# Kernel tuning notes

Measured on AMD Instinct MI355X. Metric: run time of the kernel, lower is better.

## Reference

```python
import jax, jax.numpy as jnp
import numpy as np

LATENT = 2000
N_GROUPS = 10000  # loci_count // window_size
KERNEL = 20       # window_size * 2; per-group input length is 1 so out length == KERNEL
BATCH = 128
EPS = 1e-5
SLOPE = 0.1


def setup_inputs() -> dict:
    key = jax.random.key(0)
    k1, k2, k3, k4, k5 = jax.random.split(key, 5)
    return {
        "z": jax.random.normal(k1, (BATCH, LATENT), dtype=jnp.float32),
        "W_fc": jax.random.normal(k2, (N_GROUPS, LATENT), dtype=jnp.float32) * 0.02,
        "b_fc": jax.random.normal(k3, (N_GROUPS,), dtype=jnp.float32) * 0.02,
        "gamma": jnp.ones((N_GROUPS,), dtype=jnp.float32),
        "beta": jnp.zeros((N_GROUPS,), dtype=jnp.float32),
        "conv_w": jax.random.normal(k4, (N_GROUPS, KERNEL), dtype=jnp.float32) * 0.1,
        "conv_b": jax.random.normal(k5, (N_GROUPS,), dtype=jnp.float32) * 0.02,
    }


def reference(z, W_fc, b_fc, gamma, beta, conv_w, conv_b):
    # Linear: (B, L) @ (L, G) -> (B, G)
    h = jnp.einsum("bl,gl->bg", z, W_fc) + b_fc
    # BatchNorm1d (training mode: biased batch statistics, eps=1e-5)
    mean = jnp.mean(h, axis=0)
    var = jnp.mean(jnp.square(h - mean), axis=0)
    h = (h - mean) * jax.lax.rsqrt(var + EPS) * gamma + beta
    h = jnp.where(h >= 0, h, SLOPE * h)  # LeakyReLU(0.1)
    # Grouped ConvTranspose1d with per-group input length 1 degenerates to
    # an outer product per channel: y[b,g,k] = h[b,g]*w[g,k] + b[g]
    y = h[:, :, None] * conv_w[None, :, :] + conv_b[None, :, None]  # (B, G, K)
    y = jnp.where(y >= 0, y, SLOPE * y)  # LeakyReLU(0.1)
    out = jax.nn.sigmoid(y.reshape(z.shape[0], N_GROUPS * KERNEL))
    return out
```

## Files before the change

### kernel.cpp

```cpp
#include <hip/hip_runtime.h>
#include <hip/hip_bf16.h>
#include <stdint.h>

#define BATCH 128
#define LAT   2000
#define NG    10000
#define KW    20
#define OUTW  (NG * KW)
#define EPSV  1e-5f

#define GT    64
#define BK    64
#define KSPL  8
#define KSEG  256

typedef __bf16 bf16x8 __attribute__((ext_vector_type(8)));
typedef float  f32x4  __attribute__((ext_vector_type(4)));

__device__ __forceinline__ ushort f2bf(float f) {
  uint32_t u = __builtin_bit_cast(uint32_t, f);
  u = (u + 0x7FFFu + ((u >> 16) & 1u)) >> 16;
  return (ushort)u;
}

__device__ __forceinline__ int4 pack8(const float* p) {
  float4 f0 = *(const float4*)p;
  float4 f1 = *(const float4*)(p + 4);
  int4 v;
  v.x = (int)((uint32_t)f2bf(f0.x) | ((uint32_t)f2bf(f0.y) << 16));
  v.y = (int)((uint32_t)f2bf(f0.z) | ((uint32_t)f2bf(f0.w) << 16));
  v.z = (int)((uint32_t)f2bf(f1.x) | ((uint32_t)f2bf(f1.y) << 16));
  v.w = (int)((uint32_t)f2bf(f1.z) | ((uint32_t)f2bf(f1.w) << 16));
  return v;
}

__global__ __launch_bounds__(256, 4) void convert_z_kernel(
    const float* __restrict__ zp, ushort* __restrict__ zb) {
  const int idx = (blockIdx.x * 256 + threadIdx.x) * 8;
  int4 v = pack8(zp + idx);
  *(int4*)(zb + idx) = v;
}

__global__ __launch_bounds__(256, 4) void gemm_splitk_kernel(
    const ushort* __restrict__ zb, const float* __restrict__ wp,
    float* __restrict__ hp) {
  const int tid = threadIdx.x;
  const int g0  = blockIdx.x * GT;
  const int s   = blockIdx.y;
  const int kbase = s * KSEG;
  const int klen  = (s < KSPL - 1) ? KSEG : (LAT - (KSPL - 1) * KSEG);

  __shared__ ushort As[GT * BK];
  __shared__ ushort Bs[BATCH * BK];

  const int lane = tid & 63;
  const int w    = tid >> 6;
  const int wm   = w & 1;
  const int wn   = w >> 1;
  const int q    = lane >> 4;
  const int cl   = lane & 15;

  f32x4 acc[2][4];
  const f32x4 vzero = {0.f, 0.f, 0.f, 0.f};
#pragma unroll
  for (int i = 0; i < 2; ++i)
#pragma unroll
    for (int j = 0; j < 4; ++j) acc[i][j] = vzero;

  for (int it = 0; it < KSEG / BK; ++it) {
    const int k0 = it * BK;
    __syncthreads();

#pragma unroll
    for (int i = 0; i < 2; ++i) {
      int c = i * 256 + tid;
      int r = c >> 3, sc = c & 7;
      int lk = k0 + sc * 8;
      int g  = g0 + r;
      int4 v = make_int4(0, 0, 0, 0);
      if (lk < klen && g < NG)
        v = pack8(wp + (size_t)g * LAT + kbase + lk);
      *(int4*)&As[r * BK + ((sc ^ (r & 7)) << 3)] = v;
    }
#pragma unroll
    for (int i = 0; i < 4; ++i) {
      int c = i * 256 + tid;
      int r = c >> 3, sc = c & 7;
      int lk = k0 + sc * 8;
      int4 v = make_int4(0, 0, 0, 0);
      if (lk < klen)
        v = *(const int4*)(zb + (size_t)r * LAT + kbase + lk);
      *(int4*)&Bs[r * BK + ((sc ^ (r & 7)) << 3)] = v;
    }
    __syncthreads();

#pragma unroll
    for (int kk = 0; kk < 2; ++kk) {
      int sc = kk * 4 + q;
      bf16x8 af[2], bfr[4];
#pragma unroll
      for (int mt = 0; mt < 2; ++mt) {
        int ra = wm * 32 + mt * 16 + cl;
        af[mt] = *(const bf16x8*)&As[ra * BK + ((sc ^ (ra & 7)) << 3)];
      }
#pragma unroll
      for (int nt = 0; nt < 4; ++nt) {
        int rb = wn * 64 + nt * 16 + cl;
        bfr[nt] = *(const bf16x8*)&Bs[rb * BK + ((sc ^ (rb & 7)) << 3)];
      }
#pragma unroll
      for (int mt = 0; mt < 2; ++mt)
#pragma unroll
        for (int nt = 0; nt < 4; ++nt)
          acc[mt][nt] = __builtin_amdgcn_mfma_f32_16x16x32_bf16(
              af[mt], bfr[nt], acc[mt][nt], 0, 0, 0);
    }
  }

  float* base = hp + (size_t)s * NG * BATCH;
#pragma unroll
  for (int mt = 0; mt < 2; ++mt) {
#pragma unroll
    for (int r = 0; r < 4; ++r) {
      int g = g0 + wm * 32 + mt * 16 + q * 4 + r;
      if (g < NG) {
#pragma unroll
        for (int nt = 0; nt < 4; ++nt) {
          int b = wn * 64 + nt * 16 + cl;
          base[(size_t)g * BATCH + b] = acc[mt][nt][r];
        }
      }
    }
  }
}

__global__ __launch_bounds__(256, 4) void expand_kernel(
    const float* __restrict__ hp, const float* __restrict__ gammap,
    const float* __restrict__ betap, const float* __restrict__ convwp,
    const float* __restrict__ convbp, float* __restrict__ out) {
  const int tid = threadIdx.x;
  const int g   = blockIdx.x * 8 + (tid >> 5);
  const int bc  = (tid & 31) * 4;

  float4 hv = make_float4(0.f, 0.f, 0.f, 0.f);
#pragma unroll
  for (int s = 0; s < KSPL; ++s) {
    float4 v = *(const float4*)(hp + ((size_t)s * NG + g) * BATCH + bc);
    hv.x += v.x; hv.y += v.y; hv.z += v.z; hv.w += v.w;
  }

  float sm = hv.x + hv.y + hv.z + hv.w;
  float sq = hv.x * hv.x + hv.y * hv.y + hv.z * hv.z + hv.w * hv.w;
#pragma unroll
  for (int m = 1; m < 32; m <<= 1) {
    sm += __shfl_xor(sm, m);
    sq += __shfl_xor(sq, m);
  }
  float mean = sm * (1.f / 128.f);
  float var  = sq * (1.f / 128.f) - mean * mean;
  var = (var < 0.f) ? 0.f : var;
  float inv   = __builtin_amdgcn_rsqf(var + EPSV);
  float scale = inv * gammap[g];
  float shift = betap[g] - mean * scale;
  const float cb = convbp[g];

  float wv[KW];
  {
    const float4* pw = (const float4*)(convwp + (size_t)g * KW);
#pragma unroll
    for (int j = 0; j < 5; ++j) {
      float4 f = pw[j];
      wv[4 * j] = f.x; wv[4 * j + 1] = f.y;
      wv[4 * j + 2] = f.z; wv[4 * j + 3] = f.w;
    }
  }

  float hb[4] = {hv.x, hv.y, hv.z, hv.w};
#pragma unroll
  for (int i = 0; i < 4; ++i) {
    float h = hb[i] * scale + shift;
    h = fmaxf(h, h * 0.1f);
    float4 ov[5];
#pragma unroll
    for (int j = 0; j < 5; ++j) {
      float y0 = h * wv[4 * j]     + cb;
      float y1 = h * wv[4 * j + 1] + cb;
      float y2 = h * wv[4 * j + 2] + cb;
      float y3 = h * wv[4 * j + 3] + cb;
      y0 = fmaxf(y0, y0 * 0.1f);
      y1 = fmaxf(y1, y1 * 0.1f);
      y2 = fmaxf(y2, y2 * 0.1f);
      y3 = fmaxf(y3, y3 * 0.1f);
      ov[j].x = __builtin_amdgcn_rcpf(1.f + exp2f(y0 * -1.44269504f));
      ov[j].y = __builtin_amdgcn_rcpf(1.f + exp2f(y1 * -1.44269504f));
      ov[j].z = __builtin_amdgcn_rcpf(1.f + exp2f(y2 * -1.44269504f));
      ov[j].w = __builtin_amdgcn_rcpf(1.f + exp2f(y3 * -1.44269504f));
    }
    float4* po = (float4*)(out + (size_t)(bc + i) * OUTW + (size_t)g * KW);
#pragma unroll
    for (int j = 0; j < 5; ++j) po[j] = ov[j];
  }
}

__global__ __launch_bounds__(256, 2) void fused_decoder_kernel(
    const float* __restrict__ zp, const float* __restrict__ wp,
    const float* __restrict__ gammap, const float* __restrict__ betap,
    const float* __restrict__ convwp, const float* __restrict__ convbp,
    float* __restrict__ out) {
  const int tid = threadIdx.x;
  const int g0  = blockIdx.x * 32;

  __shared__ ushort As[BATCH * BK];
  __shared__ ushort Bs[32 * BK];
  __shared__ float statS[2][2][16];
  __shared__ float statQ[2][2][16];

  const int lane = tid & 63;
  const int w    = tid >> 6;
  const int wm   = w & 1;
  const int wn   = w >> 1;
  const int q    = lane >> 4;
  const int cl   = lane & 15;

  f32x4 acc[4];
  const f32x4 vzero = {0.f, 0.f, 0.f, 0.f};
#pragma unroll
  for (int i = 0; i < 4; ++i) acc[i] = vzero;

  for (int it = 0; it < 32; ++it) {
    const int k0 = it * BK;
    __syncthreads();
#pragma unroll
    for (int i = 0; i < 4; ++i) {
      int c = i * 256 + tid;
      int r = c >> 3, sc = c & 7;
      int gk = k0 + sc * 8;
      int4 v = make_int4(0, 0, 0, 0);
      if (gk < LAT) v = pack8(zp + (size_t)r * LAT + gk);
      *(int4*)&As[r * BK + ((sc ^ (r & 7)) << 3)] = v;
    }
    {
      int r = tid >> 3, sc = tid & 7;
      int g  = g0 + r;
      int gk = k0 + sc * 8;
      int4 v = make_int4(0, 0, 0, 0);
      if (gk < LAT && g < NG) v = pack8(wp + (size_t)g * LAT + gk);
      *(int4*)&Bs[r * BK + ((sc ^ (r & 7)) << 3)] = v;
    }
    __syncthreads();
#pragma unroll
    for (int kk = 0; kk < 2; ++kk) {
      int sc = kk * 4 + q;
      bf16x8 af[4], bfr;
#pragma unroll
      for (int mt = 0; mt < 4; ++mt) {
        int ra = wm * 64 + mt * 16 + cl;
        af[mt] = *(const bf16x8*)&As[ra * BK + ((sc ^ (ra & 7)) << 3)];
      }
      {
        int rb = wn * 16 + cl;
        bfr = *(const bf16x8*)&Bs[rb * BK + ((sc ^ (rb & 7)) << 3)];
      }
#pragma unroll
      for (int mt = 0; mt < 4; ++mt)
        acc[mt] = __builtin_amdgcn_mfma_f32_16x16x32_bf16(af[mt], bfr,
                                                          acc[mt], 0, 0, 0);
    }
  }

  float s = 0.f, ss = 0.f;
#pragma unroll
  for (int mt = 0; mt < 4; ++mt)
#pragma unroll
    for (int r = 0; r < 4; ++r) {
      float v = acc[mt][r];
      s += v; ss += v * v;
    }
  s += __shfl_xor(s, 16); ss += __shfl_xor(ss, 16);
  s += __shfl_xor(s, 32); ss += __shfl_xor(ss, 32);
  if (q == 0) { statS[wm][wn][cl] = s; statQ[wm][wn][cl] = ss; }
  __syncthreads();

  const int gcol = g0 + wn * 16 + cl;
  const int gc   = (gcol < NG) ? gcol : (NG - 1);
  float S = statS[0][wn][cl] + statS[1][wn][cl];
  float Q = statQ[0][wn][cl] + statQ[1][wn][cl];
  float mean = S * (1.f / 128.f);
  float var  = Q * (1.f / 128.f) - mean * mean;
  var = (var < 0.f) ? 0.f : var;
  float inv = __builtin_amdgcn_rsqf(var + EPSV);
  float ga = gammap[gc], be = betap[gc], cb = convbp[gc];
  float wv[KW];
  {
    const float4* pw = (const float4*)(convwp + (size_t)gc * KW);
#pragma unroll
    for (int j = 0; j < 5; ++j) {
      float4 f = pw[j];
      wv[4 * j] = f.x; wv[4 * j + 1] = f.y;
      wv[4 * j + 2] = f.z; wv[4 * j + 3] = f.w;
    }
  }
  float scale = inv * ga;
  float shift = be - mean * scale;
  const bool ok = (gcol < NG);
#pragma unroll
  for (int mt = 0; mt < 4; ++mt) {
#pragma unroll
    for (int r = 0; r < 4; ++r) {
      float h = acc[mt][r] * scale + shift;
      h = fmaxf(h, h * 0.1f);
      int b = wm * 64 + mt * 16 + q * 4 + r;
      float4 ov[5];
#pragma unroll
      for (int j = 0; j < 5; ++j) {
        float y0 = h * wv[4 * j]     + cb;
        float y1 = h * wv[4 * j + 1] + cb;
        float y2 = h * wv[4 * j + 2] + cb;
        float y3 = h * wv[4 * j + 3] + cb;
        y0 = fmaxf(y0, y0 * 0.1f);
        y1 = fmaxf(y1, y1 * 0.1f);
        y2 = fmaxf(y2, y2 * 0.1f);
        y3 = fmaxf(y3, y3 * 0.1f);
        ov[j].x = __builtin_amdgcn_rcpf(1.f + exp2f(y0 * -1.44269504f));
        ov[j].y = __builtin_amdgcn_rcpf(1.f + exp2f(y1 * -1.44269504f));
        ov[j].z = __builtin_amdgcn_rcpf(1.f + exp2f(y2 * -1.44269504f));
        ov[j].w = __builtin_amdgcn_rcpf(1.f + exp2f(y3 * -1.44269504f));
      }
      if (ok) {
        float4* po = (float4*)(out + (size_t)b * OUTW + (size_t)gcol * KW);
#pragma unroll
        for (int j = 0; j < 5; ++j) po[j] = ov[j];
      }
    }
  }
}

extern "C" void kernel_launch(void* const* d_in, const int* in_sizes, int n_in,
                              void* d_out, int out_size, void* d_ws, size_t ws_size,
                              hipStream_t stream) {
  const float* z     = (const float*)d_in[0];
  const float* W     = (const float*)d_in[1];
  const float* gamma = (const float*)d_in[3];
  const float* beta  = (const float*)d_in[4];
  const float* convw = (const float*)d_in[5];
  const float* convb = (const float*)d_in[6];
  float* out = (float*)d_out;

  const size_t hp_elems = (size_t)KSPL * NG * BATCH;
  const size_t need = hp_elems * 4 + (size_t)BATCH * LAT * 2;

  if (ws_size >= need) {
    float*  hp = (float*)d_ws;
    ushort* zb = (ushort*)(hp + hp_elems);

    convert_z_kernel<<<BATCH * LAT / (256 * 8), 256, 0, stream>>>(z, zb);
    dim3 g1((NG + GT - 1) / GT, KSPL);
    gemm_splitk_kernel<<<g1, 256, 0, stream>>>(zb, W, hp);
    expand_kernel<<<NG / 8, 256, 0, stream>>>(hp, gamma, beta, convw,
                                              convb, out);
  } else {
    fused_decoder_kernel<<<(NG + 31) / 32, 256, 0, stream>>>(
        z, W, gamma, beta, convw, convb, out);
  }
}
```

Before: 232.5 us.

## Replace LDS-tiled split-K GEMM with barrier-free per-wave GEMM and bf16 partials

Rewrites the split-K GEMM so that each wavefront independently computes a 16-group by 128-batch tile over a K chunk. It loads W and bf16 z straight from global memory into MFMA operands, with no shared memory and no barriers. The split count drops from 8 to 7, and the partial sums are stored as bf16 instead of fp32, which roughly halves the partial-sum traffic written by the GEMM and read by the expand kernel. The tradeoffs are that z is re-read from global/L2 by every wave with no LDS reuse, and the bf16 partials lose accuracy before the batch-norm statistics are computed.

```diff
diff --git a/kernel.cpp b/kernel.cpp
--- a/kernel.cpp
+++ b/kernel.cpp
@@ -9,10 +9,9 @@
 #define OUTW  (NG * KW)
 #define EPSV  1e-5f
 
-#define GT    64
-#define BK    64
-#define KSPL  8
-#define KSEG  256
+#define KSPL  7
+#define CPS   9
+#define NTILE 625
 
 typedef __bf16 bf16x8 __attribute__((ext_vector_type(8)));
 typedef float  f32x4  __attribute__((ext_vector_type(4)));
@@ -21,6 +20,10 @@
   uint32_t u = __builtin_bit_cast(uint32_t, f);
   u = (u + 0x7FFFu + ((u >> 16) & 1u)) >> 16;
   return (ushort)u;
+}
+__device__ __forceinline__ float bf2f(ushort h) {
+  uint32_t u = ((uint32_t)h) << 16;
+  return __builtin_bit_cast(float, u);
 }
 
 __device__ __forceinline__ int4 pack8(const float* p) {
@@ -41,101 +44,68 @@
   *(int4*)(zb + idx) = v;
 }
 
-__global__ __launch_bounds__(256, 4) void gemm_splitk_kernel(
+__global__ __launch_bounds__(256, 4) void gemm_nobarrier_kernel(
     const ushort* __restrict__ zb, const float* __restrict__ wp,
-    float* __restrict__ hp) {
-  const int tid = threadIdx.x;
-  const int g0  = blockIdx.x * GT;
-  const int s   = blockIdx.y;
-  const int kbase = s * KSEG;
-  const int klen  = (s < KSPL - 1) ? KSEG : (LAT - (KSPL - 1) * KSEG);
-
-  __shared__ ushort As[GT * BK];
-  __shared__ ushort Bs[BATCH * BK];
-
-  const int lane = tid & 63;
-  const int w    = tid >> 6;
-  const int wm   = w & 1;
-  const int wn   = w >> 1;
+    ushort* __restrict__ hp) {
+  const int gw = (int)((blockIdx.x * 256 + threadIdx.x) >> 6);
+  if (gw >= NTILE * KSPL) return;
+  const int lane = threadIdx.x & 63;
+  const int tile = gw / KSPL;
+  const int spl  = gw - tile * KSPL;
+  const int g0   = tile * 16;
   const int q    = lane >> 4;
   const int cl   = lane & 15;
 
-  f32x4 acc[2][4];
+  f32x4 acc[8];
   const f32x4 vzero = {0.f, 0.f, 0.f, 0.f};
 #pragma unroll
-  for (int i = 0; i < 2; ++i)
-#pragma unroll
-    for (int j = 0; j < 4; ++j) acc[i][j] = vzero;
-
-  for (int it = 0; it < KSEG / BK; ++it) {
-    const int k0 = it * BK;
-    __syncthreads();
-
-#pragma unroll
-    for (int i = 0; i < 2; ++i) {
-      int c = i * 256 + tid;
-      int r = c >> 3, sc = c & 7;
-      int lk = k0 + sc * 8;
-      int g  = g0 + r;
+  for (int i = 0; i < 8; ++i) acc[i] = vzero;
+
+  const float*  wrow = wp + (size_t)(g0 + cl) * LAT;
+  const ushort* zrow = zb + (size_t)cl * LAT;
+
+#pragma unroll
+  for (int c = 0; c < CPS; ++c) {
+    const int k0 = (spl * CPS + c) * 32 + q * 8;
+    const bool valid = (k0 < LAT);
+
+    bf16x8 afr;
+    if (valid) {
+      int4 v = pack8(wrow + k0);
+      afr = *(bf16x8*)&v;
+    } else {
       int4 v = make_int4(0, 0, 0, 0);
-      if (lk < klen && g < NG)
-        v = pack8(wp + (size_t)g * LAT + kbase + lk);
-      *(int4*)&As[r * BK + ((sc ^ (r & 7)) << 3)] = v;
-    }
-#pragma unroll
-    for (int i = 0; i < 4; ++i) {
-      int c = i * 256 + tid;
-      int r = c >> 3, sc = c & 7;
-      int lk = k0 + sc * 8;
-      int4 v = make_int4(0, 0, 0, 0);
-      if (lk < klen)
-        v = *(const int4*)(zb + (size_t)r * LAT + kbase + lk);
-      *(int4*)&Bs[r * BK + ((sc ^ (r & 7)) << 3)] = v;
-    }
-    __syncthreads();
-
-#pragma unroll
-    for (int kk = 0; kk < 2; ++kk) {
-      int sc = kk * 4 + q;
-      bf16x8 af[2], bfr[4];
-#pragma unroll
-      for (int mt = 0; mt < 2; ++mt) {
-        int ra = wm * 32 + mt * 16 + cl;
-        af[mt] = *(const bf16x8*)&As[ra * BK + ((sc ^ (ra & 7)) << 3)];
-      }
-#pragma unroll
-      for (int nt = 0; nt < 4; ++nt) {
-        int rb = wn * 64 + nt * 16 + cl;
-        bfr[nt] = *(const bf16x8*)&Bs[rb * BK + ((sc ^ (rb & 7)) << 3)];
-      }
-#pragma unroll
-      for (int mt = 0; mt < 2; ++mt)
-#pragma unroll
-        for (int nt = 0; nt < 4; ++nt)
-          acc[mt][nt] = __builtin_amdgcn_mfma_f32_16x16x32_bf16(
-              af[mt], bfr[nt], acc[mt][nt], 0, 0, 0);
-    }
-  }
-
-  float* base = hp + (size_t)s * NG * BATCH;
-#pragma unroll
-  for (int mt = 0; mt < 2; ++mt) {
-#pragma unroll
-    for (int r = 0; r < 4; ++r) {
-      int g = g0 + wm * 32 + mt * 16 + q * 4 + r;
-      if (g < NG) {
-#pragma unroll
-        for (int nt = 0; nt < 4; ++nt) {
-          int b = wn * 64 + nt * 16 + cl;
-          base[(size_t)g * BATCH + b] = acc[mt][nt][r];
-        }
-      }
-    }
+      afr = *(bf16x8*)&v;
+    }
+
+    bf16x8 bfr[8];
+#pragma unroll
+    for (int nt = 0; nt < 8; ++nt) {
+      if (valid)
+        bfr[nt] = *(const bf16x8*)(zrow + (size_t)(nt * 16) * LAT + k0);
+      else {
+        int4 v = make_int4(0, 0, 0, 0);
+        bfr[nt] = *(bf16x8*)&v;
+      }
+    }
+#pragma unroll
+    for (int nt = 0; nt < 8; ++nt)
+      acc[nt] = __builtin_amdgcn_mfma_f32_16x16x32_bf16(afr, bfr[nt],
+                                                        acc[nt], 0, 0, 0);
+  }
+
+  ushort* base = hp + ((size_t)spl * NG + g0) * BATCH;
+#pragma unroll
+  for (int r = 0; r < 4; ++r) {
+    ushort* rowp = base + (size_t)(q * 4 + r) * BATCH + cl;
+#pragma unroll
+    for (int nt = 0; nt < 8; ++nt)
+      rowp[nt * 16] = f2bf(acc[nt][r]);
   }
 }
 
 __global__ __launch_bounds__(256, 4) void expand_kernel(
-    const float* __restrict__ hp, const float* __restrict__ gammap,
+    const ushort* __restrict__ hp, const float* __restrict__ gammap,
     const float* __restrict__ betap, const float* __restrict__ convwp,
     const float* __restrict__ convbp, float* __restrict__ out) {
   const int tid = threadIdx.x;
@@ -145,8 +115,9 @@
   float4 hv = make_float4(0.f, 0.f, 0.f, 0.f);
 #pragma unroll
   for (int s = 0; s < KSPL; ++s) {
-    float4 v = *(const float4*)(hp + ((size_t)s * NG + g) * BATCH + bc);
-    hv.x += v.x; hv.y += v.y; hv.z += v.z; hv.w += v.w;
+    ushort4 v = *(const ushort4*)(hp + ((size_t)s * NG + g) * BATCH + bc);
+    hv.x += bf2f(v.x); hv.y += bf2f(v.y);
+    hv.z += bf2f(v.z); hv.w += bf2f(v.w);
   }
 
   float sm = hv.x + hv.y + hv.z + hv.w;
@@ -202,6 +173,7 @@
   }
 }
 
+#define FBK 64
 __global__ __launch_bounds__(256, 2) void fused_decoder_kernel(
     const float* __restrict__ zp, const float* __restrict__ wp,
     const float* __restrict__ gammap, const float* __restrict__ betap,
@@ -210,8 +182,8 @@
   const int tid = threadIdx.x;
   const int g0  = blockIdx.x * 32;
 
-  __shared__ ushort As[BATCH * BK];
-  __shared__ ushort Bs[32 * BK];
+  __shared__ ushort As[BATCH * FBK];
+  __shared__ ushort Bs[32 * FBK];
   __shared__ float statS[2][2][16];
   __shared__ float statQ[2][2][16];
 
@@ -228,7 +200,7 @@
   for (int i = 0; i < 4; ++i) acc[i] = vzero;
 
   for (int it = 0; it < 32; ++it) {
-    const int k0 = it * BK;
+    const int k0 = it * FBK;
     __syncthreads();
 #pragma unroll
     for (int i = 0; i < 4; ++i) {
@@ -237,7 +209,7 @@
       int gk = k0 + sc * 8;
       int4 v = make_int4(0, 0, 0, 0);
       if (gk < LAT) v = pack8(zp + (size_t)r * LAT + gk);
-      *(int4*)&As[r * BK + ((sc ^ (r & 7)) << 3)] = v;
+      *(int4*)&As[r * FBK + ((sc ^ (r & 7)) << 3)] = v;
     }
     {
       int r = tid >> 3, sc = tid & 7;
@@ -245,7 +217,7 @@
       int gk = k0 + sc * 8;
       int4 v = make_int4(0, 0, 0, 0);
       if (gk < LAT && g < NG) v = pack8(wp + (size_t)g * LAT + gk);
-      *(int4*)&Bs[r * BK + ((sc ^ (r & 7)) << 3)] = v;
+      *(int4*)&Bs[r * FBK + ((sc ^ (r & 7)) << 3)] = v;
     }
     __syncthreads();
 #pragma unroll
@@ -255,11 +227,11 @@
 #pragma unroll
       for (int mt = 0; mt < 4; ++mt) {
         int ra = wm * 64 + mt * 16 + cl;
-        af[mt] = *(const bf16x8*)&As[ra * BK + ((sc ^ (ra & 7)) << 3)];
+        af[mt] = *(const bf16x8*)&As[ra * FBK + ((sc ^ (ra & 7)) << 3)];
       }
       {
         int rb = wn * 16 + cl;
-        bfr = *(const bf16x8*)&Bs[rb * BK + ((sc ^ (rb & 7)) << 3)];
+        bfr = *(const bf16x8*)&Bs[rb * FBK + ((sc ^ (rb & 7)) << 3)];
       }
 #pragma unroll
       for (int mt = 0; mt < 4; ++mt)
@@ -347,15 +319,17 @@
   float* out = (float*)d_out;
 
   const size_t hp_elems = (size_t)KSPL * NG * BATCH;
-  const size_t need = hp_elems * 4 + (size_t)BATCH * LAT * 2;
+  const size_t zb_elems = (size_t)BATCH * LAT;
+  const size_t need = (hp_elems + zb_elems) * sizeof(ushort);
 
   if (ws_size >= need) {
-    float*  hp = (float*)d_ws;
-    ushort* zb = (ushort*)(hp + hp_elems);
+    ushort* hp = (ushort*)d_ws;
+    ushort* zb = hp + hp_elems;
 
     convert_z_kernel<<<BATCH * LAT / (256 * 8), 256, 0, stream>>>(z, zb);
-    dim3 g1((NG + GT - 1) / GT, KSPL);
-    gemm_splitk_kernel<<<g1, 256, 0, stream>>>(zb, W, hp);
+    const int nwaves  = NTILE * KSPL;
+    const int nblocks = (nwaves + 3) / 4;
+    gemm_nobarrier_kernel<<<nblocks, 256, 0, stream>>>(zb, W, hp);
     expand_kernel<<<NG / 8, 256, 0, stream>>>(hp, gamma, beta, convw,
                                               convb, out);
   } else {
```

Result: slower. 248.5 us (+6.9%).
